# Kernel optimization log

Hardware: AMD Instinct MI355X
Metric: run time of the kernel (lower is better)

The kernel has to match this reference:

```python
import jax, jax.numpy as jnp
import numpy as np

# Config matching GConv(in_channels=64, out_channels=64, kernel_type=1,
#                       is_first=False, rot_1x1_in=False, stride=1, padding=1, dilation=1)
KERNEL_TYPE = 1
NUM_KERNEL = 9      # taps per sparse kernel
KERNEL_ROT = 4      # number of rotations
STEP = 8 // KERNEL_ROT
STRIDE, PAD, DIL = 1, 1, 1
CIN, COUT = 64, 64

# Ring of the 8 neighbor offsets (dy, dx) in 45-degree steps around the center.
RING = [(-1, -1), (-1, 0), (-1, 1), (0, 1), (1, 1), (1, 0), (1, -1), (0, -1)]

def tap_offsets(kernel_type, rot8):
    """Tap positions of the sparse 3x3 kernel, rotated by rot8 * 45 degrees."""
    if kernel_type == 1:      # full 3x3: center + 8 ring taps
        ring_ids = list(range(8))
    elif kernel_type == 0:    # skeleton: center + 4-cross
        ring_ids = [0, 2, 4, 6]
    else:                     # bar: center + opposite pair
        ring_ids = [0, 4]
    return [(0, 0)] + [RING[(i + rot8) % 8] for i in ring_ids]


def sparse_spatial_conv(x, w, offs):
    """x: [N, C, H, W], w: [O, C, T], offs: T tap offsets.
    Each tap contributes its own output-channel group (no tap summation):
    returns [N, T*O, Ho, Wo] with tap-major channel ordering (matches torch.cat)."""
    N, C, H, W = x.shape
    Ho = (H + 2 * PAD - (DIL * 2 + 1)) // STRIDE + 1
    Wo = (W + 2 * PAD - (DIL * 2 + 1)) // STRIDE + 1
    xp = jnp.pad(x, ((0, 0), (0, 0), (PAD, PAD), (PAD, PAD)))
    shifts = []
    for dy, dx in offs:
        sh, sw = (dy + 1) * DIL, (dx + 1) * DIL
        shifts.append(xp[:, :, sh:sh + (Ho - 1) * STRIDE + 1:STRIDE,
                             sw:sw + (Wo - 1) * STRIDE + 1:STRIDE])
    xs = jnp.stack(shifts, axis=0)               # [T, N, C, Ho, Wo]
    out = jnp.einsum('tnchw,oct->tnohw', xs, w)  # per-tap 1x1 conv at shifted pos
    Tt = out.shape[0]
    return out.transpose(1, 0, 2, 3, 4).reshape(N, Tt * w.shape[0], Ho, Wo)


def setup_inputs() -> dict:
    key = jax.random.key(0)
    k1, k2 = jax.random.split(key)
    x_tensor = jax.random.normal(k1, (8, CIN, KERNEL_ROT, 64, 64), dtype=jnp.float32)
    weight = jax.random.normal(k2, (COUT, CIN, KERNEL_ROT, NUM_KERNEL), dtype=jnp.float32) * 0.05
    return {"x_tensor": x_tensor, "weight": weight}


def reference(x_tensor, weight):
    N, Cin, R, H, W = x_tensor.shape
    # cat rotation dim into channels (rot-major): [N, R*Cin, H, W]
    x_cat = x_tensor.transpose(0, 2, 1, 3, 4).reshape(N, R * Cin, H, W)
    O = weight.shape[0]
    rot_out = []
    for rot in range(KERNEL_ROT):
        # rotated weight gather: cat weight[:, :, (idx - rot) % R, :] over idx along dim=1
        idxs = (np.arange(R) - rot) % R
        w_rot = weight[:, :, idxs, :]                    # [O, Cin, R, T]
        w_rot = w_rot.transpose(0, 2, 1, 3).reshape(O, R * Cin, NUM_KERNEL)
        offs = tap_offsets(KERNEL_TYPE, STEP * rot)
        rot_out.append(sparse_spatial_conv(x_cat, w_rot, offs))  # [N, T*O, Ho, Wo]
    return jnp.stack(rot_out, axis=2)  # [N, T*O, R, Ho, Wo]
```

## Files before the change

kernel.cpp:

```cpp
#include <hip/hip_runtime.h>
#include <stdint.h>

using short8 = __attribute__((ext_vector_type(8))) short;
using f32x4  = __attribute__((ext_vector_type(4))) float;

__device__ __forceinline__ unsigned short f2bf(float f) {
    unsigned int u = __float_as_uint(f);
    unsigned int r = (u + 0x7fffu + ((u >> 16) & 1u)) >> 16;
    return (unsigned short)r;
}

__global__ __launch_bounds__(256) void k_zero(unsigned short* __restrict__ xt) {
    int idx = blockIdx.x * 256 + threadIdx.x;
    int n = idx >> 12; int rr = (idx >> 11) & 1; int cpos = idx & 2047;
    f32x4 z = {0.f, 0.f, 0.f, 0.f};
    *(f32x4*)((char*)xt + (size_t)(n * 66 + (rr ? 65 : 0)) * 32768 + cpos * 16) = z;
}

__global__ __launch_bounds__(256) void k_xpose(const float* __restrict__ x,
                                               unsigned short* __restrict__ xt) {
    __shared__ unsigned short sm[256][72];
    int b = blockIdx.x; int n = b >> 6; int h = b & 63;
    int tid = threadIdx.x;
    int c = tid >> 2, r = tid & 3; int k = r * 64 + c;
    const float* src = x + ((((size_t)n * 64 + c) * 4 + r) * 64 + h) * 64;
#pragma unroll
    for (int i = 0; i < 64; i += 4) {
        float4 v = *(const float4*)(src + i);
        sm[k][i + 0] = f2bf(v.x); sm[k][i + 1] = f2bf(v.y);
        sm[k][i + 2] = f2bf(v.z); sm[k][i + 3] = f2bf(v.w);
    }
    __syncthreads();
    int w = tid & 63, kg = tid >> 6;
    unsigned short* dst = xt + ((size_t)(n * 66 + (h + 1)) * 64 + w) * 256;
    int key = (w + 1) & 7;
#pragma unroll
    for (int cc = 0; cc < 8; cc++) {
        int s = kg * 8 + cc; int sp = s ^ key;
        short8 v;
#pragma unroll
        for (int e = 0; e < 8; e++) v[e] = (short)sm[s * 8 + e][w];
        *(short8*)(dst + sp * 8) = v;
    }
}

__global__ __launch_bounds__(256) void k_wprep(const float* __restrict__ wgt,
                                               unsigned short* __restrict__ ball) {
    int idx = blockIdx.x * 256 + threadIdx.x;
    int k = idx & 255; int col = (idx >> 8) & 255; int j = idx >> 16;
    int rot = col >> 6, o = col & 63;
    int r = k >> 6, c = k & 63;
    int t = (j == 0) ? 0 : (1 + ((j - 1 - 2 * rot) & 7));
    float v = wgt[((o * 64 + c) * 4 + ((r - rot) & 3)) * 9 + t];
    ball[idx] = f2bf(v);
}

__global__ __launch_bounds__(512) void k_main(const unsigned short* __restrict__ xt,
                                              const unsigned short* __restrict__ ball,
                                              float* __restrict__ out) {
    extern __shared__ char lds[];
    int blk = blockIdx.x; int n = blk >> 5; int h0 = (blk & 31) * 2;
    int tid = threadIdx.x;

    const char* xbase = (const char*)xt;
#pragma unroll
    for (int i = 0; i < 16; i++) {
        int chunk = tid + i * 512;
        int r4 = chunk >> 11; int cin = chunk & 2047;
        short8 v = *(const short8*)(xbase + (size_t)(n * 66 + h0 + r4) * 32768 + cin * 16);
        *(short8*)(lds + r4 * 33792 + 512 + cin * 16) = v;
    }
    if (tid < 256) {
        int r4 = tid >> 6; int sp = (tid >> 5) & 1; int cc = tid & 31;
        f32x4 z = {0.f, 0.f, 0.f, 0.f};
        *(f32x4*)(lds + r4 * 33792 + (sp ? 65 * 512 : 0) + cc * 16) = z;
    }
    __syncthreads();

    int wv = tid >> 6; int l = tid & 63; int l15 = l & 15; int l4 = l >> 4;
    int rot = wv >> 1;
    const char* bb = (const char*)ball;

    for (int j = 0; j < 9; j++) {
        int dy = ((0x1A901 >> (2 * j)) & 3) - 1;
        int dx = ((0x01A91 >> (2 * j)) & 3) - 1;
        int t = (j == 0) ? 0 : (1 + ((j - 1 - 2 * rot) & 7));

        short8 Bf[2][8];
#pragma unroll
        for (int ct = 0; ct < 2; ct++) {
            int col = wv * 32 + ct * 16 + l15;
            const char* bp = bb + j * 131072 + col * 512 + l4 * 16;
#pragma unroll
            for (int ks = 0; ks < 8; ks++) Bf[ct][ks] = *(const short8*)(bp + ks * 64);
        }

#pragma unroll 1
        for (int mtp = 0; mtp < 4; mtp++) {
            short8 Af[2][8];
#pragma unroll
            for (int m2 = 0; m2 < 2; m2++) {
                int mt = mtp * 2 + m2;
                int pixel = mt * 16 + l15;
                int r4 = (pixel >> 6) + dy + 1;
                int ws = (pixel & 63) + dx + 1;
                const char* ap = lds + (r4 * 66 + ws) * 512;
                int key = ws & 7;
#pragma unroll
                for (int ks = 0; ks < 8; ks++) {
                    int s = ks * 4 + l4;
                    Af[m2][ks] = *(const short8*)(ap + ((s ^ key) << 4));
                }
            }
            f32x4 acc[2][2];
#pragma unroll
            for (int a = 0; a < 2; a++)
#pragma unroll
                for (int b2 = 0; b2 < 2; b2++) acc[a][b2] = (f32x4){0.f, 0.f, 0.f, 0.f};
#pragma unroll
            for (int ks = 0; ks < 8; ks++)
#pragma unroll
                for (int ct = 0; ct < 2; ct++)
#pragma unroll
                    for (int m2 = 0; m2 < 2; m2++)
                        acc[ct][m2] = __builtin_amdgcn_mfma_f32_16x16x32_bf16(
                            Af[m2][ks], Bf[ct][ks], acc[ct][m2], 0, 0, 0);
#pragma unroll
            for (int ct = 0; ct < 2; ct++) {
                int o = (wv & 1) * 32 + ct * 16 + l15;
#pragma unroll
                for (int m2 = 0; m2 < 2; m2++) {
                    int mt = mtp * 2 + m2;
                    int pb = mt * 16 + 4 * l4;
                    int h = h0 + (mt >> 2);
                    int wb = pb & 63;
                    int idx = (((n * 576 + t * 64 + o) * 4 + rot) * 64 + h) * 64 + wb;
                    *(f32x4*)(out + idx) = acc[ct][m2];
                }
            }
        }
    }
}

__global__ __launch_bounds__(256) void k_naive(const float* __restrict__ x,
                                               const float* __restrict__ wgt,
                                               float* __restrict__ out) {
    int idx = blockIdx.x * 256 + threadIdx.x;
    if (idx >= 75497472) return;
    int w = idx & 63, h = (idx >> 6) & 63, rot = (idx >> 12) & 3;
    int chn = idx >> 14; int ch = chn % 576; int n = chn / 576;
    int t = ch >> 6, o = ch & 63;
    int dy = 0, dx = 0;
    if (t > 0) {
        int ri = (t - 1 + 2 * rot) & 7;
        dy = ((27200 >> (2 * ri)) & 3) - 1;
        dx = ((1700 >> (2 * ri)) & 3) - 1;
    }
    int hh = h + dy, ww = w + dx;
    float acc = 0.f;
    if (hh >= 0 && hh < 64 && ww >= 0 && ww < 64) {
        for (int r = 0; r < 4; r++) {
            int rr = (r - rot) & 3;
            for (int c = 0; c < 64; c++)
                acc += x[(((n * 64 + c) * 4 + r) * 64 + hh) * 64 + ww] *
                       wgt[((o * 64 + c) * 4 + rr) * 9 + t];
        }
    }
    out[idx] = acc;
}

extern "C" void kernel_launch(void* const* d_in, const int* in_sizes, int n_in,
                              void* d_out, int out_size, void* d_ws, size_t ws_size,
                              hipStream_t stream) {
    const float* x = (const float*)d_in[0];
    const float* wgt = (const float*)d_in[1];
    float* out = (float*)d_out;
    const size_t XT_BYTES = (size_t)8 * 66 * 64 * 256 * 2;
    const size_t NEED = XT_BYTES + (size_t)9 * 256 * 256 * 2;
    if (ws_size < NEED) {
        k_naive<<<(75497472 + 255) / 256, 256, 0, stream>>>(x, wgt, out);
        return;
    }
    unsigned short* xt = (unsigned short*)d_ws;
    unsigned short* ball = (unsigned short*)((char*)d_ws + XT_BYTES);
    k_zero<<<128, 256, 0, stream>>>(xt);
    k_xpose<<<512, 256, 0, stream>>>(x, xt);
    k_wprep<<<2304, 256, 0, stream>>>(wgt, ball);
    k_main<<<256, 512, 135168, stream>>>(xt, ball, out);
}
```

Baseline: 98.14 us.

## Merge prep kernels and retile main GEMM per wave over rot and row

Folds the zero-padding, transpose and weight-prep kernels into a single launch with block-range dispatch, removing two kernel launches. In the main kernel each wave now owns one rotation and one output row and computes all 64 output channels, loading weights in two K halves and reusing them across 4 pixel tiles, instead of reloading per 32-column slice. Output uses nontemporal stores and input uses nontemporal loads to reduce cache pollution. The larger accumulator tile (16 f32x4) raises register pressure.

New measurement: 126.9 us. 29.3% more time.

```diff
diff --git a/kernel.cpp b/kernel.cpp
--- a/kernel.cpp
+++ b/kernel.cpp
@@ -10,49 +10,49 @@
     return (unsigned short)r;
 }
 
-__global__ __launch_bounds__(256) void k_zero(unsigned short* __restrict__ xt) {
-    int idx = blockIdx.x * 256 + threadIdx.x;
-    int n = idx >> 12; int rr = (idx >> 11) & 1; int cpos = idx & 2047;
-    f32x4 z = {0.f, 0.f, 0.f, 0.f};
-    *(f32x4*)((char*)xt + (size_t)(n * 66 + (rr ? 65 : 0)) * 32768 + cpos * 16) = z;
-}
-
-__global__ __launch_bounds__(256) void k_xpose(const float* __restrict__ x,
-                                               unsigned short* __restrict__ xt) {
+__global__ __launch_bounds__(256) void k_prep(const float* __restrict__ x,
+                                              const float* __restrict__ wgt,
+                                              unsigned short* __restrict__ xt,
+                                              unsigned short* __restrict__ ball) {
     __shared__ unsigned short sm[256][72];
-    int b = blockIdx.x; int n = b >> 6; int h = b & 63;
+    int b = blockIdx.x;
     int tid = threadIdx.x;
-    int c = tid >> 2, r = tid & 3; int k = r * 64 + c;
-    const float* src = x + ((((size_t)n * 64 + c) * 4 + r) * 64 + h) * 64;
+    if (b < 512) {
+        int n = b >> 6; int h = b & 63;
+        int c = tid >> 2, r = tid & 3; int k = r * 64 + c;
+        const float* src = x + ((((size_t)n * 64 + c) * 4 + r) * 64 + h) * 64;
 #pragma unroll
-    for (int i = 0; i < 64; i += 4) {
-        float4 v = *(const float4*)(src + i);
-        sm[k][i + 0] = f2bf(v.x); sm[k][i + 1] = f2bf(v.y);
-        sm[k][i + 2] = f2bf(v.z); sm[k][i + 3] = f2bf(v.w);
+        for (int i = 0; i < 64; i += 4) {
+            f32x4 v = __builtin_nontemporal_load((const f32x4*)(src + i));
+            sm[k][i + 0] = f2bf(v[0]); sm[k][i + 1] = f2bf(v[1]);
+            sm[k][i + 2] = f2bf(v[2]); sm[k][i + 3] = f2bf(v[3]);
+        }
+        __syncthreads();
+        int w = tid & 63, kg = tid >> 6;
+        unsigned short* dst = xt + ((size_t)(n * 66 + (h + 1)) * 64 + w) * 256;
+        int key = (w + 1) & 7;
+#pragma unroll
+        for (int cc = 0; cc < 8; cc++) {
+            int s = kg * 8 + cc; int sp = s ^ key;
+            short8 v;
+#pragma unroll
+            for (int e = 0; e < 8; e++) v[e] = (short)sm[s * 8 + e][w];
+            *(short8*)(dst + sp * 8) = v;
+        }
+    } else if (b < 640) {
+        int idx = (b - 512) * 256 + tid;
+        int n = idx >> 12; int rr = (idx >> 11) & 1; int cpos = idx & 2047;
+        f32x4 z = {0.f, 0.f, 0.f, 0.f};
+        *(f32x4*)((char*)xt + (size_t)(n * 66 + (rr ? 65 : 0)) * 32768 + cpos * 16) = z;
+    } else {
+        int idx = (b - 640) * 256 + tid;
+        int k = idx & 255; int col = (idx >> 8) & 255; int j = idx >> 16;
+        int rot = col >> 6, o = col & 63;
+        int r = k >> 6, c = k & 63;
+        int t = (j == 0) ? 0 : (1 + ((j - 1 - 2 * rot) & 7));
+        float v = wgt[((o * 64 + c) * 4 + ((r - rot) & 3)) * 9 + t];
+        ball[idx] = f2bf(v);
     }
-    __syncthreads();
-    int w = tid & 63, kg = tid >> 6;
-    unsigned short* dst = xt + ((size_t)(n * 66 + (h + 1)) * 64 + w) * 256;
-    int key = (w + 1) & 7;
-#pragma unroll
-    for (int cc = 0; cc < 8; cc++) {
-        int s = kg * 8 + cc; int sp = s ^ key;
-        short8 v;
-#pragma unroll
-        for (int e = 0; e < 8; e++) v[e] = (short)sm[s * 8 + e][w];
-        *(short8*)(dst + sp * 8) = v;
-    }
-}
-
-__global__ __launch_bounds__(256) void k_wprep(const float* __restrict__ wgt,
-                                               unsigned short* __restrict__ ball) {
-    int idx = blockIdx.x * 256 + threadIdx.x;
-    int k = idx & 255; int col = (idx >> 8) & 255; int j = idx >> 16;
-    int rot = col >> 6, o = col & 63;
-    int r = k >> 6, c = k & 63;
-    int t = (j == 0) ? 0 : (1 + ((j - 1 - 2 * rot) & 7));
-    float v = wgt[((o * 64 + c) * 4 + ((r - rot) & 3)) * 9 + t];
-    ball[idx] = f2bf(v);
 }
 
 __global__ __launch_bounds__(512) void k_main(const unsigned short* __restrict__ xt,
@@ -78,65 +78,66 @@
     __syncthreads();
 
     int wv = tid >> 6; int l = tid & 63; int l15 = l & 15; int l4 = l >> 4;
-    int rot = wv >> 1;
-    const char* bb = (const char*)ball;
+    int rot = wv & 3; int mhalf = wv >> 2;
+    int h = h0 + mhalf;
 
+#pragma unroll 1
     for (int j = 0; j < 9; j++) {
         int dy = ((0x1A901 >> (2 * j)) & 3) - 1;
         int dx = ((0x01A91 >> (2 * j)) & 3) - 1;
         int t = (j == 0) ? 0 : (1 + ((j - 1 - 2 * rot) & 7));
+        int r4 = mhalf + dy + 1;
+        const char* arow = lds + r4 * 33792;
 
-        short8 Bf[2][8];
+        f32x4 acc[4][4];
 #pragma unroll
-        for (int ct = 0; ct < 2; ct++) {
-            int col = wv * 32 + ct * 16 + l15;
-            const char* bp = bb + j * 131072 + col * 512 + l4 * 16;
+        for (int a = 0; a < 4; a++)
 #pragma unroll
-            for (int ks = 0; ks < 8; ks++) Bf[ct][ks] = *(const short8*)(bp + ks * 64);
-        }
+            for (int b2 = 0; b2 < 4; b2++) acc[a][b2] = (f32x4){0.f, 0.f, 0.f, 0.f};
 
 #pragma unroll 1
-        for (int mtp = 0; mtp < 4; mtp++) {
-            short8 Af[2][8];
+        for (int kh = 0; kh < 2; kh++) {
+            short8 Bf[4][4];
 #pragma unroll
-            for (int m2 = 0; m2 < 2; m2++) {
-                int mt = mtp * 2 + m2;
-                int pixel = mt * 16 + l15;
-                int r4 = (pixel >> 6) + dy + 1;
-                int ws = (pixel & 63) + dx + 1;
-                const char* ap = lds + (r4 * 66 + ws) * 512;
-                int key = ws & 7;
+            for (int ct = 0; ct < 4; ct++) {
+                const char* bp = (const char*)ball + j * 131072 +
+                                 (rot * 64 + ct * 16 + l15) * 512 + kh * 256 + l4 * 16;
 #pragma unroll
-                for (int ks = 0; ks < 8; ks++) {
-                    int s = ks * 4 + l4;
-                    Af[m2][ks] = *(const short8*)(ap + ((s ^ key) << 4));
-                }
+                for (int ks = 0; ks < 4; ks++) Bf[ct][ks] = *(const short8*)(bp + ks * 64);
             }
-            f32x4 acc[2][2];
 #pragma unroll
-            for (int a = 0; a < 2; a++)
-#pragma unroll
-                for (int b2 = 0; b2 < 2; b2++) acc[a][b2] = (f32x4){0.f, 0.f, 0.f, 0.f};
-#pragma unroll
-            for (int ks = 0; ks < 8; ks++)
-#pragma unroll
-                for (int ct = 0; ct < 2; ct++)
-#pragma unroll
-                    for (int m2 = 0; m2 < 2; m2++)
-                        acc[ct][m2] = __builtin_amdgcn_mfma_f32_16x16x32_bf16(
-                            Af[m2][ks], Bf[ct][ks], acc[ct][m2], 0, 0, 0);
-#pragma unroll
-            for (int ct = 0; ct < 2; ct++) {
-                int o = (wv & 1) * 32 + ct * 16 + l15;
+            for (int mtp = 0; mtp < 2; mtp++) {
+                short8 Af[2][4];
 #pragma unroll
                 for (int m2 = 0; m2 < 2; m2++) {
-                    int mt = mtp * 2 + m2;
-                    int pb = mt * 16 + 4 * l4;
-                    int h = h0 + (mt >> 2);
-                    int wb = pb & 63;
-                    int idx = (((n * 576 + t * 64 + o) * 4 + rot) * 64 + h) * 64 + wb;
-                    *(f32x4*)(out + idx) = acc[ct][m2];
+                    int pw = (mtp * 2 + m2) * 16 + l15;
+                    int ws = pw + dx + 1;
+                    const char* ap = arow + ws * 512;
+                    int key = ws & 7;
+#pragma unroll
+                    for (int ks = 0; ks < 4; ks++) {
+                        int s = kh * 16 + ks * 4 + l4;
+                        Af[m2][ks] = *(const short8*)(ap + ((s ^ key) << 4));
+                    }
                 }
+#pragma unroll
+                for (int ks = 0; ks < 4; ks++)
+#pragma unroll
+                    for (int ct = 0; ct < 4; ct++)
+#pragma unroll
+                        for (int m2 = 0; m2 < 2; m2++)
+                            acc[mtp * 2 + m2][ct] = __builtin_amdgcn_mfma_f32_16x16x32_bf16(
+                                Af[m2][ks], Bf[ct][ks], acc[mtp * 2 + m2][ct], 0, 0, 0);
+            }
+        }
+        size_t ob = ((size_t)n * 2304 + (size_t)t * 256 + rot) * 4096 + (size_t)h * 64;
+#pragma unroll
+        for (int ct = 0; ct < 4; ct++) {
+            int o = ct * 16 + l15;
+#pragma unroll
+            for (int ml = 0; ml < 4; ml++) {
+                int wb = ml * 16 + 4 * l4;
+                __builtin_nontemporal_store(acc[ml][ct], (f32x4*)(out + ob + (size_t)o * 16384 + wb));
             }
         }
     }
@@ -183,8 +184,6 @@
     }
     unsigned short* xt = (unsigned short*)d_ws;
     unsigned short* ball = (unsigned short*)((char*)d_ws + XT_BYTES);
-    k_zero<<<128, 256, 0, stream>>>(xt);
-    k_xpose<<<512, 256, 0, stream>>>(x, xt);
-    k_wprep<<<2304, 256, 0, stream>>>(wgt, ball);
+    k_prep<<<2944, 256, 0, stream>>>(x, wgt, xt, ball);
     k_main<<<256, 512, 135168, stream>>>(xt, ball, out);
 }
```

## Fuse input transpose and bf16 conversion into main conv kernel

Applied to the files above, without the earlier changes.

Removes the separate zero-fill and transpose kernels and the bf16 staging buffer in the workspace. The main kernel now reads fp32 input directly, converts it to bf16 and transposes it through an extra LDS staging area into the swizzled pixel-major layout, and zero-fills out-of-range halo rows in place. Block indices are also remapped so that consecutive blocks are spread across different rows and images. This saves two launches and a global round trip, but puts strided fp32 loads and extra barriers at the start of every block. Each block reads halo rows that neighbouring blocks also read, and the larger LDS footprint may limit occupancy.

New measurement: 83.84 us. -14.6%, faster.

```diff
diff --git a/kernel.cpp b/kernel.cpp
--- a/kernel.cpp
+++ b/kernel.cpp
@@ -8,40 +8,6 @@
     unsigned int u = __float_as_uint(f);
     unsigned int r = (u + 0x7fffu + ((u >> 16) & 1u)) >> 16;
     return (unsigned short)r;
-}
-
-__global__ __launch_bounds__(256) void k_zero(unsigned short* __restrict__ xt) {
-    int idx = blockIdx.x * 256 + threadIdx.x;
-    int n = idx >> 12; int rr = (idx >> 11) & 1; int cpos = idx & 2047;
-    f32x4 z = {0.f, 0.f, 0.f, 0.f};
-    *(f32x4*)((char*)xt + (size_t)(n * 66 + (rr ? 65 : 0)) * 32768 + cpos * 16) = z;
-}
-
-__global__ __launch_bounds__(256) void k_xpose(const float* __restrict__ x,
-                                               unsigned short* __restrict__ xt) {
-    __shared__ unsigned short sm[256][72];
-    int b = blockIdx.x; int n = b >> 6; int h = b & 63;
-    int tid = threadIdx.x;
-    int c = tid >> 2, r = tid & 3; int k = r * 64 + c;
-    const float* src = x + ((((size_t)n * 64 + c) * 4 + r) * 64 + h) * 64;
-#pragma unroll
-    for (int i = 0; i < 64; i += 4) {
-        float4 v = *(const float4*)(src + i);
-        sm[k][i + 0] = f2bf(v.x); sm[k][i + 1] = f2bf(v.y);
-        sm[k][i + 2] = f2bf(v.z); sm[k][i + 3] = f2bf(v.w);
-    }
-    __syncthreads();
-    int w = tid & 63, kg = tid >> 6;
-    unsigned short* dst = xt + ((size_t)(n * 66 + (h + 1)) * 64 + w) * 256;
-    int key = (w + 1) & 7;
-#pragma unroll
-    for (int cc = 0; cc < 8; cc++) {
-        int s = kg * 8 + cc; int sp = s ^ key;
-        short8 v;
-#pragma unroll
-        for (int e = 0; e < 8; e++) v[e] = (short)sm[s * 8 + e][w];
-        *(short8*)(dst + sp * 8) = v;
-    }
 }
 
 __global__ __launch_bounds__(256) void k_wprep(const float* __restrict__ wgt,
@@ -55,27 +21,60 @@
     ball[idx] = f2bf(v);
 }
 
-__global__ __launch_bounds__(512) void k_main(const unsigned short* __restrict__ xt,
+__global__ __launch_bounds__(512) void k_main(const float* __restrict__ x,
                                               const unsigned short* __restrict__ ball,
                                               float* __restrict__ out) {
     extern __shared__ char lds[];
-    int blk = blockIdx.x; int n = blk >> 5; int h0 = (blk & 31) * 2;
+    int d = blockIdx.x;
+    int orig = (d & 7) * 32 + (d >> 3);
+    int n = orig >> 5; int h0 = (orig & 31) * 2;
     int tid = threadIdx.x;
+    unsigned short* smu = (unsigned short*)(lds + 135168);
 
-    const char* xbase = (const char*)xt;
-#pragma unroll
-    for (int i = 0; i < 16; i++) {
-        int chunk = tid + i * 512;
-        int r4 = chunk >> 11; int cin = chunk & 2047;
-        short8 v = *(const short8*)(xbase + (size_t)(n * 66 + h0 + r4) * 32768 + cin * 16);
-        *(short8*)(lds + r4 * 33792 + 512 + cin * 16) = v;
-    }
     if (tid < 256) {
         int r4 = tid >> 6; int sp = (tid >> 5) & 1; int cc = tid & 31;
         f32x4 z = {0.f, 0.f, 0.f, 0.f};
         *(f32x4*)(lds + r4 * 33792 + (sp ? 65 * 512 : 0) + cc * 16) = z;
     }
-    __syncthreads();
+
+    int wA = tid & 63; int kq = tid >> 6;
+#pragma unroll 1
+    for (int r4 = 0; r4 < 4; r4++) {
+        int hh = h0 - 1 + r4;
+        bool ok = ((unsigned)hh < 64u);
+#pragma unroll 1
+        for (int half = 0; half < 2; half++) {
+            if (ok) {
+#pragma unroll
+                for (int e = 0; e < 16; e++) {
+                    int kl = kq * 16 + e;
+                    int k = half * 128 + kl;
+                    int r = k >> 6, c = k & 63;
+                    float v = x[(((n * 64 + c) * 4 + r) * 64 + hh) * 64 + wA];
+                    smu[kl * 66 + wA] = f2bf(v);
+                }
+            } else {
+#pragma unroll
+                for (int e = 0; e < 16; e++) smu[(kq * 16 + e) * 66 + wA] = 0;
+            }
+            __syncthreads();
+            {
+                int w = tid & 63; int q = tid >> 6;
+                int key = (w + 1) & 7;
+                char* prow = lds + (r4 * 66 + (w + 1)) * 512;
+#pragma unroll
+                for (int ss = 0; ss < 2; ss++) {
+                    int sl = q + ss * 8;
+                    int sg = half * 16 + sl;
+                    short8 vv;
+#pragma unroll
+                    for (int e = 0; e < 8; e++) vv[e] = (short)smu[(sl * 8 + e) * 66 + w];
+                    *(short8*)(prow + ((sg ^ key) << 4)) = vv;
+                }
+            }
+            __syncthreads();
+        }
+    }
 
     int wv = tid >> 6; int l = tid & 63; int l15 = l & 15; int l4 = l >> 4;
     int rot = wv >> 1;
@@ -175,16 +174,12 @@
     const float* x = (const float*)d_in[0];
     const float* wgt = (const float*)d_in[1];
     float* out = (float*)d_out;
-    const size_t XT_BYTES = (size_t)8 * 66 * 64 * 256 * 2;
-    const size_t NEED = XT_BYTES + (size_t)9 * 256 * 256 * 2;
+    const size_t NEED = (size_t)9 * 256 * 256 * 2;
     if (ws_size < NEED) {
         k_naive<<<(75497472 + 255) / 256, 256, 0, stream>>>(x, wgt, out);
         return;
     }
-    unsigned short* xt = (unsigned short*)d_ws;
-    unsigned short* ball = (unsigned short*)((char*)d_ws + XT_BYTES);
-    k_zero<<<128, 256, 0, stream>>>(xt);
-    k_xpose<<<512, 256, 0, stream>>>(x, xt);
+    unsigned short* ball = (unsigned short*)d_ws;
     k_wprep<<<2304, 256, 0, stream>>>(wgt, ball);
-    k_main<<<256, 512, 135168, stream>>>(xt, ball, out);
+    k_main<<<256, 512, 152064, stream>>>(x, ball, out);
 }
```
